# Optimization experiments

Hardware: AMD Instinct MI355X
Metric: run time of the kernel (lower is better)

## Reference

```python
import jax, jax.numpy as jnp
import numpy as np

N_NODES = 100000
N_EDGES = 3200000
IN_CH = 512
HIDDEN = 64
LOC_OUT = 16
OUT_CH = 40


def setup_inputs() -> dict:
    key = jax.random.key(0)
    ks = jax.random.split(key, 10)
    return {
        "batch_x": jax.random.normal(ks[0], (N_NODES, IN_CH), dtype=jnp.float32),
        "edge_index": jax.random.randint(ks[1], (2, N_EDGES), 0, N_NODES, dtype=jnp.int64),
        "glob_emb": jax.random.normal(ks[2], (N_NODES, LOC_OUT), dtype=jnp.float32),
        "W1": jax.random.normal(ks[3], (IN_CH, HIDDEN), dtype=jnp.float32) * (1.0 / np.sqrt(IN_CH)),
        "b1": jnp.zeros((HIDDEN,), dtype=jnp.float32),
        "W2": jax.random.normal(ks[4], (HIDDEN, LOC_OUT), dtype=jnp.float32) * (1.0 / np.sqrt(HIDDEN)),
        "b2": jnp.zeros((LOC_OUT,), dtype=jnp.float32),
        "att_w1": jax.random.normal(ks[5], (LOC_OUT, 16), dtype=jnp.float32) * 0.25,
        "att_b1": jnp.zeros((16,), dtype=jnp.float32),
        "att_w2": jax.random.normal(ks[6], (16, 1), dtype=jnp.float32) * 0.25,
        "lin1_w": jax.random.normal(ks[7], (LOC_OUT, OUT_CH), dtype=jnp.float32) * 0.25,
        "lin1_b": jnp.zeros((OUT_CH,), dtype=jnp.float32),
    }


def _gcn_conv(x, W, b, row, col, n):
    # GCNConv: out = D^-1/2 (A + I) D^-1/2 (X W) + b   (PyG default: self-loops, sym norm)
    h = x @ W
    loops = jnp.arange(n, dtype=row.dtype)
    row2 = jnp.concatenate([row, loops])  # sources (x_j)
    col2 = jnp.concatenate([col, loops])  # targets (aggregation index)
    deg = jax.ops.segment_sum(jnp.ones_like(col2, dtype=h.dtype), col2, num_segments=n)
    dinv = jax.lax.rsqrt(jnp.maximum(deg, 1.0))  # deg >= 1 thanks to self-loops
    norm = dinv[row2] * dinv[col2]               # [E+N]
    agg = jax.ops.segment_sum(h[row2] * norm[:, None], col2, num_segments=n)
    return agg + b


def reference(batch_x, edge_index, glob_emb, W1, b1, W2, b2, att_w1, att_b1, att_w2, lin1_w, lin1_b):
    n = batch_x.shape[0]
    row, col = edge_index[0], edge_index[1]
    x = _gcn_conv(batch_x, W1, b1, row, col, n)
    x = jax.nn.relu(x)  # dropout p=0.0 -> identity
    x = _gcn_conv(x, W2, b2, row, col, n)  # last layer: no relu/dropout
    z = jnp.stack([x, glob_emb], axis=1)  # [N, 2, 16]
    w = jnp.tanh(z @ att_w1 + att_b1) @ att_w2  # [N, 2, 1]
    beta = jax.nn.softmax(w, axis=1)
    emb = jnp.sum(beta * z, axis=1)  # [N, 16]
    return emb @ lin1_w + lin1_b  # [N, 40]
```

## Files before the change

kernel.cpp:

```cpp
#include <hip/hip_runtime.h>

#define N_IN 512
#define HID 64
#define NBLK 256
#define TILE 2048

typedef __attribute__((ext_vector_type(4))) float f32x4;
typedef __attribute__((ext_vector_type(8))) short bf16x8;

__device__ inline float bf2f(unsigned short s) {
    union { unsigned int u; float f; } v; v.u = ((unsigned int)s) << 16; return v.f;
}
__device__ inline unsigned short f2bf(float f) {
    union { float f; unsigned int u; } v; v.f = f;
    unsigned int u = v.u;
    return (unsigned short)((u + 0x7FFFu + ((u >> 16) & 1u)) >> 16);
}

__global__ __launch_bounds__(256) void k_histA_wt(const int* __restrict__ EI, int* __restrict__ hist,
                                                  const float* __restrict__ W1, unsigned short* __restrict__ Wt,
                                                  int E, int N, int K) {
    if (blockIdx.x >= NBLK) {
        int i = (blockIdx.x - NBLK) * 256 + threadIdx.x;
        int k = i >> 6, n = i & 63;
        Wt[n * 512 + k] = f2bf(W1[i]);
        return;
    }
    __shared__ int hs[512];
    __shared__ int sflag;
    if (threadIdx.x == 0) sflag = (EI[1] == 0 && EI[3] == 0 && EI[5] == 0 && EI[7] == 0) ? 1 : 0;
    for (int k = threadIdx.x; k < 512; k += 256) hs[k] = 0;
    __syncthreads();
    bool f = sflag != 0;
    int chunk = (E + NBLK - 1) / NBLK;
    int s = blockIdx.x * chunk, e = min(E, s + chunk);
    for (int i = s + threadIdx.x; i < e; i += 256) {
        int c = f ? ((const int2*)EI)[E + i].x : EI[E + i];
        if ((unsigned)c < (unsigned)N) atomicAdd(&hs[c >> 8], 1);
    }
    __syncthreads();
    for (int k = threadIdx.x; k < K; k += 256) hist[k * NBLK + blockIdx.x] = hs[k];
}

__global__ __launch_bounds__(256) void k_scan_a2(int* __restrict__ data, int* __restrict__ bsum, int n) {
    __shared__ int sd[256];
    int i = blockIdx.x * 256 + threadIdx.x;
    int v = (i < n) ? data[i] : 0;
    sd[threadIdx.x] = v;
    __syncthreads();
    for (int off = 1; off < 256; off <<= 1) {
        int t = 0;
        if (threadIdx.x >= (unsigned)off) t = sd[threadIdx.x - off];
        __syncthreads();
        sd[threadIdx.x] += t;
        __syncthreads();
    }
    if (i < n) data[i] = sd[threadIdx.x] - v;
    if (threadIdx.x == 255) bsum[blockIdx.x] = sd[255];
}

__global__ __launch_bounds__(512) void k_scan_b(const int* __restrict__ bsum, int* __restrict__ bexc, int nb) {
    __shared__ int sd[512];
    int t = threadIdx.x;
    int v = (t < nb) ? bsum[t] : 0;
    sd[t] = v;
    __syncthreads();
    for (int off = 1; off < 512; off <<= 1) {
        int u = 0;
        if (t >= off) u = sd[t - off];
        __syncthreads();
        sd[t] += u;
        __syncthreads();
    }
    if (t < nb) bexc[t] = sd[t] - v;
    if (t == 511) bexc[nb] = sd[511];
}

__global__ __launch_bounds__(256) void k_partB(const int* __restrict__ EI, const int* __restrict__ hist,
                                               const int* __restrict__ bexc, int* __restrict__ edges2,
                                               int E, int N, int K) {
    __shared__ int val[TILE];
    __shared__ unsigned short bkt[TILE];
    __shared__ int sorted[TILE];
    __shared__ unsigned short sbkt[TILE];
    __shared__ int cnt[512], seg[512], cur[512], gcur[512];
    __shared__ int wsum[4];
    __shared__ int sflag;
    int tid = threadIdx.x, b = blockIdx.x;
    int lane = tid & 63, wv = tid >> 6;
    if (tid == 0) sflag = (EI[1] == 0 && EI[3] == 0 && EI[5] == 0 && EI[7] == 0) ? 1 : 0;
    for (int k = tid; k < 512; k += 256) gcur[k] = (k < K) ? (bexc[k] + hist[k * NBLK + b]) : 0;
    __syncthreads();
    bool f = sflag != 0;
    int chunk = (E + NBLK - 1) / NBLK;
    int s = b * chunk, e = min(E, s + chunk);
    for (int ts = s; ts < e; ts += TILE) {
        int n = min(e - ts, TILE);
        for (int k = tid; k < 512; k += 256) cnt[k] = 0;
        __syncthreads();
        for (int i = tid; i < n; i += 256) {
            int r, c;
            if (f) { const int2* E2 = (const int2*)EI; r = E2[ts + i].x; c = E2[E + ts + i].x; }
            else   { r = EI[ts + i]; c = EI[E + ts + i]; }
            if ((unsigned)c < (unsigned)N) {
                unsigned short kb = (unsigned short)(c >> 8);
                if ((unsigned)r >= (unsigned)N) r = 0;
                val[i] = r | ((c & 255) << 20);
                bkt[i] = kb;
                atomicAdd(&cnt[kb], 1);
            } else bkt[i] = 0xFFFFu;
        }
        __syncthreads();
        int v0 = cnt[2 * tid], v1 = cnt[2 * tid + 1];
        int p = v0 + v1, pi = p;
        for (int d = 1; d < 64; d <<= 1) {
            int u = __shfl_up(pi, d, 64);
            if (lane >= d) pi += u;
        }
        if (lane == 63) wsum[wv] = pi;
        __syncthreads();
        int woff = 0, tot = 0;
        for (int q = 0; q < 4; ++q) { int t2 = wsum[q]; if (q < wv) woff += t2; tot += t2; }
        int pe = woff + pi - p;
        seg[2 * tid] = pe; seg[2 * tid + 1] = pe + v0;
        cur[2 * tid] = pe; cur[2 * tid + 1] = pe + v0;
        __syncthreads();
        for (int i = tid; i < n; i += 256) {
            unsigned short kb = bkt[i];
            if (kb != 0xFFFFu) {
                int pos = atomicAdd(&cur[kb], 1);
                sorted[pos] = val[i];
                sbkt[pos] = kb;
            }
        }
        __syncthreads();
        for (int j = tid; j < tot; j += 256) {
            int kb = sbkt[j];
            edges2[gcur[kb] + (j - seg[kb])] = sorted[j];
        }
        __syncthreads();
        for (int k = tid; k < K; k += 256) gcur[k] += cnt[k];
        __syncthreads();
    }
}

__global__ __launch_bounds__(256) void k_gemm1(const float* __restrict__ X, const unsigned short* __restrict__ Wt,
                                               unsigned short* __restrict__ H, int N) {
    int tid = threadIdx.x;
    int w = tid >> 6, lane = tid & 63;
    int m_l = lane & 15, q = lane >> 4;
    int m0 = blockIdx.x * 128 + w * 32;
    int rA0 = m0 + m_l, rA1 = m0 + 16 + m_l;
    int rc0 = rA0 < N ? rA0 : N - 1;
    int rc1 = rA1 < N ? rA1 : N - 1;
    const float* baseA0 = X + (size_t)rc0 * 512 + q * 8;
    const float* baseA1 = X + (size_t)rc1 * 512 + q * 8;
    const unsigned short* baseB = Wt + (size_t)m_l * 512 + q * 8;

    f32x4 acc[2][4] = {};
#pragma unroll 4
    for (int c = 0; c < 16; ++c) {
        int ko = c * 32;
        float4 x0a = *(const float4*)(baseA0 + ko);
        float4 x0b = *(const float4*)(baseA0 + ko + 4);
        float4 x1a = *(const float4*)(baseA1 + ko);
        float4 x1b = *(const float4*)(baseA1 + ko + 4);
        bf16x8 a0, a1;
        a0[0] = (short)f2bf(x0a.x); a0[1] = (short)f2bf(x0a.y); a0[2] = (short)f2bf(x0a.z); a0[3] = (short)f2bf(x0a.w);
        a0[4] = (short)f2bf(x0b.x); a0[5] = (short)f2bf(x0b.y); a0[6] = (short)f2bf(x0b.z); a0[7] = (short)f2bf(x0b.w);
        a1[0] = (short)f2bf(x1a.x); a1[1] = (short)f2bf(x1a.y); a1[2] = (short)f2bf(x1a.z); a1[3] = (short)f2bf(x1a.w);
        a1[4] = (short)f2bf(x1b.x); a1[5] = (short)f2bf(x1b.y); a1[6] = (short)f2bf(x1b.z); a1[7] = (short)f2bf(x1b.w);
#pragma unroll
        for (int t = 0; t < 4; ++t) {
            bf16x8 bb = *(const bf16x8*)(baseB + (size_t)t * 16 * 512 + ko);
            acc[0][t] = __builtin_amdgcn_mfma_f32_16x16x32_bf16(a0, bb, acc[0][t], 0, 0, 0);
            acc[1][t] = __builtin_amdgcn_mfma_f32_16x16x32_bf16(a1, bb, acc[1][t], 0, 0, 0);
        }
    }
#pragma unroll
    for (int h = 0; h < 2; ++h) {
#pragma unroll
        for (int rg = 0; rg < 4; ++rg) {
            int row = m0 + h * 16 + q * 4 + rg;
            if (row < N) {
#pragma unroll
                for (int t = 0; t < 4; ++t)
                    H[(size_t)row * 64 + t * 16 + m_l] = f2bf(acc[h][t][rg]);
            }
        }
    }
}

__global__ __launch_bounds__(256) void k_bucket(const int* __restrict__ bexc, const int* __restrict__ edges2,
                                                int* __restrict__ edges, int* __restrict__ start,
                                                float* __restrict__ dinv, unsigned short* __restrict__ H,
                                                int N, int K) {
    __shared__ int hist[256], sd[256], cur[256];
    __shared__ float dvs[256];
    int b = blockIdx.x, tid = threadIdx.x;
    int base = bexc[b];
    int end  = bexc[b + 1];
    hist[tid] = 0;
    __syncthreads();
    for (int i = base + tid; i < end; i += 256)
        atomicAdd(&hist[(edges2[i] >> 20) & 255], 1);
    __syncthreads();
    int v = hist[tid];
    sd[tid] = v;
    __syncthreads();
    for (int off = 1; off < 256; off <<= 1) {
        int t = 0;
        if (tid >= off) t = sd[tid - off];
        __syncthreads();
        sd[tid] += t;
        __syncthreads();
    }
    int excl = sd[tid] - v;
    cur[tid] = excl;
    int node = b * 256 + tid;
    float dvv = rsqrtf((float)(v + 1));
    dvs[tid] = dvv;
    if (node < N) {
        start[node] = base + excl;
        dinv[node] = dvv;
    }
    if (b == 0 && tid == 0) start[N] = bexc[K];
    __syncthreads();
    for (int i = base + tid; i < end; i += 256) {
        int pv = edges2[i];
        int pos = atomicAdd(&cur[(pv >> 20) & 255], 1);
        edges[base + pos] = pv & 0xFFFFF;
    }
    for (int rr = tid >> 4; rr < 256; rr += 16) {
        int n2 = b * 256 + rr;
        if (n2 < N) {
            float dv2 = dvs[rr];
            uint2* pp = (uint2*)(H + (size_t)n2 * 64 + (size_t)(tid & 15) * 4);
            uint2 vv = *pp;
            float f0 = bf2f((unsigned short)(vv.x & 0xffffu)) * dv2;
            float f1 = bf2f((unsigned short)(vv.x >> 16)) * dv2;
            float f2 = bf2f((unsigned short)(vv.y & 0xffffu)) * dv2;
            float f3 = bf2f((unsigned short)(vv.y >> 16)) * dv2;
            vv.x = (unsigned int)f2bf(f0) | ((unsigned int)f2bf(f1) << 16);
            vv.y = (unsigned int)f2bf(f2) | ((unsigned int)f2bf(f3) << 16);
            *pp = vv;
        }
    }
}

__global__ __launch_bounds__(256) void k_agg1g2(const unsigned short* __restrict__ H, const int* __restrict__ edges,
                                                const int* __restrict__ start, const float* __restrict__ dinv,
                                                const float* __restrict__ b1, const float* __restrict__ W2,
                                                unsigned short* __restrict__ H2, int N) {
    __shared__ float w2s[64 * 17];
    int tid = threadIdx.x;
    for (int i = tid; i < 1024; i += 256) { int k = i >> 4, c = i & 15; w2s[k * 17 + c] = W2[i]; }
    __syncthreads();
    int wid = blockIdx.x * 4 + (tid >> 6);
    int lane = tid & 63;
    if (wid >= N) return;
    int g = lane >> 4;
    int c4 = lane & 15;
    const size_t coff = (size_t)c4 * 4;
    float a0 = 0.f, a1 = 0.f, a2 = 0.f, a3 = 0.f;
    int s = start[wid], e = start[wid + 1];
    int i = s;
    if ((i & 3) && i < e) {
        int lim = min(e, (i + 3) & ~3);
        int j = i + g;
        if (j < lim) {
            uint2 v = *(const uint2*)(H + (size_t)edges[j] * 64 + coff);
            a0 += __uint_as_float(v.x << 16);
            a1 += __uint_as_float(v.x & 0xffff0000u);
            a2 += __uint_as_float(v.y << 16);
            a3 += __uint_as_float(v.y & 0xffff0000u);
        }
        i = lim;
    }
    for (; i + 32 <= e; i += 32) {
        int4 s0 = *(const int4*)(edges + i + g * 4);
        int4 s1 = *(const int4*)(edges + i + 16 + g * 4);
        uint2 v0 = *(const uint2*)(H + (size_t)s0.x * 64 + coff);
        uint2 v1 = *(const uint2*)(H + (size_t)s0.y * 64 + coff);
        uint2 v2 = *(const uint2*)(H + (size_t)s0.z * 64 + coff);
        uint2 v3 = *(const uint2*)(H + (size_t)s0.w * 64 + coff);
        uint2 v4 = *(const uint2*)(H + (size_t)s1.x * 64 + coff);
        uint2 v5 = *(const uint2*)(H + (size_t)s1.y * 64 + coff);
        uint2 v6 = *(const uint2*)(H + (size_t)s1.z * 64 + coff);
        uint2 v7 = *(const uint2*)(H + (size_t)s1.w * 64 + coff);
        a0 += __uint_as_float(v0.x << 16) + __uint_as_float(v1.x << 16)
            + __uint_as_float(v2.x << 16) + __uint_as_float(v3.x << 16)
            + __uint_as_float(v4.x << 16) + __uint_as_float(v5.x << 16)
            + __uint_as_float(v6.x << 16) + __uint_as_float(v7.x << 16);
        a1 += __uint_as_float(v0.x & 0xffff0000u) + __uint_as_float(v1.x & 0xffff0000u)
            + __uint_as_float(v2.x & 0xffff0000u) + __uint_as_float(v3.x & 0xffff0000u)
            + __uint_as_float(v4.x & 0xffff0000u) + __uint_as_float(v5.x & 0xffff0000u)
            + __uint_as_float(v6.x & 0xffff0000u) + __uint_as_float(v7.x & 0xffff0000u);
        a2 += __uint_as_float(v0.y << 16) + __uint_as_float(v1.y << 16)
            + __uint_as_float(v2.y << 16) + __uint_as_float(v3.y << 16)
            + __uint_as_float(v4.y << 16) + __uint_as_float(v5.y << 16)
            + __uint_as_float(v6.y << 16) + __uint_as_float(v7.y << 16);
        a3 += __uint_as_float(v0.y & 0xffff0000u) + __uint_as_float(v1.y & 0xffff0000u)
            + __uint_as_float(v2.y & 0xffff0000u) + __uint_as_float(v3.y & 0xffff0000u)
            + __uint_as_float(v4.y & 0xffff0000u) + __uint_as_float(v5.y & 0xffff0000u)
            + __uint_as_float(v6.y & 0xffff0000u) + __uint_as_float(v7.y & 0xffff0000u);
    }
    if (i + 16 <= e) {
        int4 sv = *(const int4*)(edges + i + g * 4);
        uint2 v0 = *(const uint2*)(H + (size_t)sv.x * 64 + coff);
        uint2 v1 = *(const uint2*)(H + (size_t)sv.y * 64 + coff);
        uint2 v2 = *(const uint2*)(H + (size_t)sv.z * 64 + coff);
        uint2 v3 = *(const uint2*)(H + (size_t)sv.w * 64 + coff);
        a0 += __uint_as_float(v0.x << 16) + __uint_as_float(v1.x << 16)
            + __uint_as_float(v2.x << 16) + __uint_as_float(v3.x << 16);
        a1 += __uint_as_float(v0.x & 0xffff0000u) + __uint_as_float(v1.x & 0xffff0000u)
            + __uint_as_float(v2.x & 0xffff0000u) + __uint_as_float(v3.x & 0xffff0000u);
        a2 += __uint_as_float(v0.y << 16) + __uint_as_float(v1.y << 16)
            + __uint_as_float(v2.y << 16) + __uint_as_float(v3.y << 16);
        a3 += __uint_as_float(v0.y & 0xffff0000u) + __uint_as_float(v1.y & 0xffff0000u)
            + __uint_as_float(v2.y & 0xffff0000u) + __uint_as_float(v3.y & 0xffff0000u);
        i += 16;
    }
    for (; i < e; i += 4) {
        int j = i + g;
        if (j < e) {
            uint2 v = *(const uint2*)(H + (size_t)edges[j] * 64 + coff);
            a0 += __uint_as_float(v.x << 16);
            a1 += __uint_as_float(v.x & 0xffff0000u);
            a2 += __uint_as_float(v.y << 16);
            a3 += __uint_as_float(v.y & 0xffff0000u);
        }
    }
    a0 += __shfl_xor(a0, 16, 64); a0 += __shfl_xor(a0, 32, 64);
    a1 += __shfl_xor(a1, 16, 64); a1 += __shfl_xor(a1, 32, 64);
    a2 += __shfl_xor(a2, 16, 64); a2 += __shfl_xor(a2, 32, 64);
    a3 += __shfl_xor(a3, 16, 64); a3 += __shfl_xor(a3, 32, 64);
    float dv = dinv[wid];
    uint2 sv = *(const uint2*)(H + (size_t)wid * 64 + coff);
    a0 += __uint_as_float(sv.x << 16);
    a1 += __uint_as_float(sv.x & 0xffff0000u);
    a2 += __uint_as_float(sv.y << 16);
    a3 += __uint_as_float(sv.y & 0xffff0000u);
    float4 bv = *(const float4*)(b1 + c4 * 4);
    float r0 = fmaxf(a0 * dv + bv.x, 0.f);
    float r1 = fmaxf(a1 * dv + bv.y, 0.f);
    float r2 = fmaxf(a2 * dv + bv.z, 0.f);
    float r3 = fmaxf(a3 * dv + bv.w, 0.f);
    float p = 0.f;
#pragma unroll
    for (int j = 0; j < 4; ++j) {
        int src = 4 * g + j;
        float x0 = __shfl(r0, src, 64);
        float x1 = __shfl(r1, src, 64);
        float x2 = __shfl(r2, src, 64);
        float x3 = __shfl(r3, src, 64);
        int kb = 16 * g + 4 * j;
        p += x0 * w2s[(kb + 0) * 17 + c4];
        p += x1 * w2s[(kb + 1) * 17 + c4];
        p += x2 * w2s[(kb + 2) * 17 + c4];
        p += x3 * w2s[(kb + 3) * 17 + c4];
    }
    p += __shfl_xor(p, 16, 64);
    p += __shfl_xor(p, 32, 64);
    if (g == 0) H2[(size_t)wid * 16 + c4] = f2bf(p * dv);
}

__global__ __launch_bounds__(256) void k_agg2(const unsigned short* __restrict__ H2, const int* __restrict__ edges,
                                              const int* __restrict__ start, const float* __restrict__ dinv,
                                              const float* __restrict__ b2, float* __restrict__ X2, int N) {
    int wid = blockIdx.x * 4 + (threadIdx.x >> 6);
    int lane = threadIdx.x & 63;
    if (wid >= N) return;
    int g = lane >> 3;
    int c2 = lane & 7;
    const size_t coff = (size_t)c2 * 2;
    float a0 = 0.f, a1 = 0.f;
    int s = start[wid], e = start[wid + 1];
    int i = s;
    if ((i & 3) && i < e) {
        int lim = min(e, (i + 3) & ~3);
        int j = i + g;
        if (j < lim) {
            unsigned int v = *(const unsigned int*)(H2 + (size_t)edges[j] * 16 + coff);
            a0 += __uint_as_float(v << 16);
            a1 += __uint_as_float(v & 0xffff0000u);
        }
        i = lim;
    }
    for (; i + 64 <= e; i += 64) {
        int4 s0 = *(const int4*)(edges + i + g * 4);
        int4 s1 = *(const int4*)(edges + i + 32 + g * 4);
        unsigned int v0 = *(const unsigned int*)(H2 + (size_t)s0.x * 16 + coff);
        unsigned int v1 = *(const unsigned int*)(H2 + (size_t)s0.y * 16 + coff);
        unsigned int v2 = *(const unsigned int*)(H2 + (size_t)s0.z * 16 + coff);
        unsigned int v3 = *(const unsigned int*)(H2 + (size_t)s0.w * 16 + coff);
        unsigned int v4 = *(const unsigned int*)(H2 + (size_t)s1.x * 16 + coff);
        unsigned int v5 = *(const unsigned int*)(H2 + (size_t)s1.y * 16 + coff);
        unsigned int v6 = *(const unsigned int*)(H2 + (size_t)s1.z * 16 + coff);
        unsigned int v7 = *(const unsigned int*)(H2 + (size_t)s1.w * 16 + coff);
        a0 += __uint_as_float(v0 << 16) + __uint_as_float(v1 << 16)
            + __uint_as_float(v2 << 16) + __uint_as_float(v3 << 16)
            + __uint_as_float(v4 << 16) + __uint_as_float(v5 << 16)
            + __uint_as_float(v6 << 16) + __uint_as_float(v7 << 16);
        a1 += __uint_as_float(v0 & 0xffff0000u) + __uint_as_float(v1 & 0xffff0000u)
            + __uint_as_float(v2 & 0xffff0000u) + __uint_as_float(v3 & 0xffff0000u)
            + __uint_as_float(v4 & 0xffff0000u) + __uint_as_float(v5 & 0xffff0000u)
            + __uint_as_float(v6 & 0xffff0000u) + __uint_as_float(v7 & 0xffff0000u);
    }
    if (i + 32 <= e) {
        int4 sv = *(const int4*)(edges + i + g * 4);
        unsigned int v0 = *(const unsigned int*)(H2 + (size_t)sv.x * 16 + coff);
        unsigned int v1 = *(const unsigned int*)(H2 + (size_t)sv.y * 16 + coff);
        unsigned int v2 = *(const unsigned int*)(H2 + (size_t)sv.z * 16 + coff);
        unsigned int v3 = *(const unsigned int*)(H2 + (size_t)sv.w * 16 + coff);
        a0 += __uint_as_float(v0 << 16) + __uint_as_float(v1 << 16)
            + __uint_as_float(v2 << 16) + __uint_as_float(v3 << 16);
        a1 += __uint_as_float(v0 & 0xffff0000u) + __uint_as_float(v1 & 0xffff0000u)
            + __uint_as_float(v2 & 0xffff0000u) + __uint_as_float(v3 & 0xffff0000u);
        i += 32;
    }
    for (; i < e; i += 8) {
        int j = i + g;
        if (j < e) {
            unsigned int v = *(const unsigned int*)(H2 + (size_t)edges[j] * 16 + coff);
            a0 += __uint_as_float(v << 16);
            a1 += __uint_as_float(v & 0xffff0000u);
        }
    }
    a0 += __shfl_xor(a0, 8, 64); a0 += __shfl_xor(a0, 16, 64); a0 += __shfl_xor(a0, 32, 64);
    a1 += __shfl_xor(a1, 8, 64); a1 += __shfl_xor(a1, 16, 64); a1 += __shfl_xor(a1, 32, 64);
    if (g == 0) {
        float dv = dinv[wid];
        unsigned int sv = *(const unsigned int*)(H2 + (size_t)wid * 16 + coff);
        a0 += __uint_as_float(sv << 16);
        a1 += __uint_as_float(sv & 0xffff0000u);
        float2 bv = *(const float2*)(b2 + c2 * 2);
        float2 o; o.x = a0 * dv + bv.x; o.y = a1 * dv + bv.y;
        *(float2*)(X2 + (size_t)wid * 16 + coff) = o;
    }
}

__global__ __launch_bounds__(256) void k_head(const float* __restrict__ X2, const float* __restrict__ G,
                                              const float* __restrict__ AW1, const float* __restrict__ AB1,
                                              const float* __restrict__ AW2, const float* __restrict__ LW,
                                              const float* __restrict__ LB, float* __restrict__ OUT, int N) {
    __shared__ float s_aw1[256], s_ab1[16], s_aw2[16], s_lw[640], s_lb[40];
    int tid = threadIdx.x;
    s_aw1[tid] = AW1[tid];
    if (tid < 16) { s_ab1[tid] = AB1[tid]; s_aw2[tid] = AW2[tid]; }
    for (int i = tid; i < 640; i += 256) s_lw[i] = LW[i];
    if (tid < 40) s_lb[tid] = LB[tid];
    __syncthreads();
    int node = blockIdx.x * 256 + tid;
    if (node >= N) return;
    float x[16], g[16];
    const float4* xp = (const float4*)(X2 + (size_t)node * 16);
    const float4* gp = (const float4*)(G + (size_t)node * 16);
#pragma unroll
    for (int q = 0; q < 4; ++q) {
        float4 v = xp[q]; x[q*4] = v.x; x[q*4+1] = v.y; x[q*4+2] = v.z; x[q*4+3] = v.w;
        float4 u = gp[q]; g[q*4] = u.x; g[q*4+1] = u.y; g[q*4+2] = u.z; g[q*4+3] = u.w;
    }
    float wx = 0.f, wg = 0.f;
#pragma unroll
    for (int j = 0; j < 16; ++j) {
        float tx = s_ab1[j], tg = s_ab1[j];
#pragma unroll
        for (int c = 0; c < 16; ++c) { tx += x[c] * s_aw1[c*16 + j]; tg += g[c] * s_aw1[c*16 + j]; }
        wx += tanhf(tx) * s_aw2[j];
        wg += tanhf(tg) * s_aw2[j];
    }
    float m = fmaxf(wx, wg);
    float ex = expf(wx - m), eg = expf(wg - m);
    float inv = 1.f / (ex + eg);
    float bx = ex * inv, bg = eg * inv;
    float emb[16];
#pragma unroll
    for (int c = 0; c < 16; ++c) emb[c] = bx * x[c] + bg * g[c];
    float* op = OUT + (size_t)node * 40;
    for (int o = 0; o < 40; ++o) {
        float a = s_lb[o];
#pragma unroll
        for (int c = 0; c < 16; ++c) a += emb[c] * s_lw[c*40 + o];
        op[o] = a;
    }
}

extern "C" void kernel_launch(void* const* d_in, const int* in_sizes, int n_in,
                              void* d_out, int out_size, void* d_ws, size_t ws_size,
                              hipStream_t stream) {
    const float* X   = (const float*)d_in[0];
    const int*   EI  = (const int*)d_in[1];
    const float* G   = (const float*)d_in[2];
    const float* W1  = (const float*)d_in[3];
    const float* B1  = (const float*)d_in[4];
    const float* W2  = (const float*)d_in[5];
    const float* B2  = (const float*)d_in[6];
    const float* AW1 = (const float*)d_in[7];
    const float* AB1 = (const float*)d_in[8];
    const float* AW2 = (const float*)d_in[9];
    const float* LW  = (const float*)d_in[10];
    const float* LB  = (const float*)d_in[11];
    float* OUT = (float*)d_out;

    const int N = in_sizes[0] / N_IN;
    const int E = in_sizes[1] / 2;
    const int NB = (N + 255) / 256;
    const int K  = NB;
    const int NH = K * NBLK;
    const int SB = (NH + 255) / 256;
    const int WB = (N_IN * HID + 255) / 256;
    const int GB = (N + 127) / 128;

    char* w = (char*)d_ws;
    size_t off = 0;
    auto take = [&](size_t bytes) -> void* {
        void* p = (void*)(w + off);
        off = (off + bytes + 255) & ~(size_t)255;
        return p;
    };
    int*   hist   = (int*)take((size_t)NH * 4);
    int*   bsum   = (int*)take((size_t)SB * 4);
    int*   bexc   = (int*)take((size_t)(SB + 1) * 4);
    int*   startp = (int*)take((size_t)(N + 1) * 4);
    float* dinvp  = (float*)take((size_t)N * 4);
    int*   edges2 = (int*)take((size_t)E * 4);
    int*   edges  = (int*)take((size_t)E * 4);
    unsigned short* wt = (unsigned short*)take((size_t)N_IN * HID * 2);
    unsigned short* h1 = (unsigned short*)take((size_t)N * 64 * 2);
    unsigned short* h2 = (unsigned short*)take((size_t)N * 16 * 2);
    float* x2 = (float*)take((size_t)N * 16 * 4);
    (void)ws_size; (void)n_in; (void)out_size;

    k_histA_wt<<<NBLK + WB, 256, 0, stream>>>(EI, hist, W1, wt, E, N, K);
    k_scan_a2 <<<SB, 256, 0, stream>>>(hist, bsum, NH);
    k_scan_b  <<<1, 512, 0, stream>>>(bsum, bexc, SB);
    k_partB   <<<NBLK, 256, 0, stream>>>(EI, hist, bexc, edges2, E, N, K);
    k_gemm1   <<<GB, 256, 0, stream>>>(X, wt, h1, N);
    k_bucket  <<<K, 256, 0, stream>>>(bexc, edges2, edges, startp, dinvp, h1, N, K);
    k_agg1g2  <<<(N + 3) / 4, 256, 0, stream>>>(h1, edges, startp, dinvp, B1, W2, h2, N);
    k_agg2    <<<(N + 3) / 4, 256, 0, stream>>>(h2, edges, startp, dinvp, B2, x2, N);
    k_head    <<<NB, 256, 0, stream>>>(x2, G, AW1, AB1, AW2, LW, LB, OUT, N);
}
```

Baseline: 613.1 us.

## Replace tiled local sort in edge partition with direct atomic scatter

```diff
diff --git a/kernel.cpp b/kernel.cpp
--- a/kernel.cpp
+++ b/kernel.cpp
@@ -3,7 +3,6 @@
 #define N_IN 512
 #define HID 64
 #define NBLK 256
-#define TILE 2048
 
 typedef __attribute__((ext_vector_type(4))) float f32x4;
 typedef __attribute__((ext_vector_type(8))) short bf16x8;
@@ -17,29 +16,32 @@
     return (unsigned short)((u + 0x7FFFu + ((u >> 16) & 1u)) >> 16);
 }
 
-__global__ __launch_bounds__(256) void k_histA_wt(const int* __restrict__ EI, int* __restrict__ hist,
-                                                  const float* __restrict__ W1, unsigned short* __restrict__ Wt,
-                                                  int E, int N, int K) {
+__global__ __launch_bounds__(1024) void k_histA_wt(const int* __restrict__ EI, int* __restrict__ hist,
+                                                   const float* __restrict__ W1, unsigned short* __restrict__ Wt,
+                                                   int E, int N, int K) {
+    int tid = threadIdx.x;
     if (blockIdx.x >= NBLK) {
-        int i = (blockIdx.x - NBLK) * 256 + threadIdx.x;
-        int k = i >> 6, n = i & 63;
-        Wt[n * 512 + k] = f2bf(W1[i]);
+        int i = (blockIdx.x - NBLK) * 1024 + tid;
+        if (i < N_IN * HID) {
+            int k = i >> 6, n = i & 63;
+            Wt[n * 512 + k] = f2bf(W1[i]);
+        }
         return;
     }
     __shared__ int hs[512];
     __shared__ int sflag;
-    if (threadIdx.x == 0) sflag = (EI[1] == 0 && EI[3] == 0 && EI[5] == 0 && EI[7] == 0) ? 1 : 0;
-    for (int k = threadIdx.x; k < 512; k += 256) hs[k] = 0;
+    if (tid == 0) sflag = (EI[1] == 0 && EI[3] == 0 && EI[5] == 0 && EI[7] == 0) ? 1 : 0;
+    if (tid < 512) hs[tid] = 0;
     __syncthreads();
     bool f = sflag != 0;
     int chunk = (E + NBLK - 1) / NBLK;
     int s = blockIdx.x * chunk, e = min(E, s + chunk);
-    for (int i = s + threadIdx.x; i < e; i += 256) {
+    for (int i = s + tid; i < e; i += 1024) {
         int c = f ? ((const int2*)EI)[E + i].x : EI[E + i];
         if ((unsigned)c < (unsigned)N) atomicAdd(&hs[c >> 8], 1);
     }
     __syncthreads();
-    for (int k = threadIdx.x; k < K; k += 256) hist[k * NBLK + blockIdx.x] = hs[k];
+    for (int k = tid; k < K; k += 1024) hist[k * NBLK + blockIdx.x] = hs[k];
 }
 
 __global__ __launch_bounds__(256) void k_scan_a2(int* __restrict__ data, int* __restrict__ bsum, int n) {
@@ -76,71 +78,25 @@
     if (t == 511) bexc[nb] = sd[511];
 }
 
-__global__ __launch_bounds__(256) void k_partB(const int* __restrict__ EI, const int* __restrict__ hist,
-                                               const int* __restrict__ bexc, int* __restrict__ edges2,
-                                               int E, int N, int K) {
-    __shared__ int val[TILE];
-    __shared__ unsigned short bkt[TILE];
-    __shared__ int sorted[TILE];
-    __shared__ unsigned short sbkt[TILE];
-    __shared__ int cnt[512], seg[512], cur[512], gcur[512];
-    __shared__ int wsum[4];
+__global__ __launch_bounds__(1024) void k_partB(const int* __restrict__ EI, const int* __restrict__ hist,
+                                                const int* __restrict__ bexc, int* __restrict__ edges2,
+                                                int E, int N, int K) {
+    __shared__ int cur[512];
     __shared__ int sflag;
     int tid = threadIdx.x, b = blockIdx.x;
-    int lane = tid & 63, wv = tid >> 6;
     if (tid == 0) sflag = (EI[1] == 0 && EI[3] == 0 && EI[5] == 0 && EI[7] == 0) ? 1 : 0;
-    for (int k = tid; k < 512; k += 256) gcur[k] = (k < K) ? (bexc[k] + hist[k * NBLK + b]) : 0;
+    if (tid < 512) cur[tid] = (tid < K) ? (bexc[tid] + hist[tid * NBLK + b]) : 0;
     __syncthreads();
     bool f = sflag != 0;
     int chunk = (E + NBLK - 1) / NBLK;
     int s = b * chunk, e = min(E, s + chunk);
-    for (int ts = s; ts < e; ts += TILE) {
-        int n = min(e - ts, TILE);
-        for (int k = tid; k < 512; k += 256) cnt[k] = 0;
-        __syncthreads();
-        for (int i = tid; i < n; i += 256) {
-            int r, c;
-            if (f) { const int2* E2 = (const int2*)EI; r = E2[ts + i].x; c = E2[E + ts + i].x; }
-            else   { r = EI[ts + i]; c = EI[E + ts + i]; }
-            if ((unsigned)c < (unsigned)N) {
-                unsigned short kb = (unsigned short)(c >> 8);
-                if ((unsigned)r >= (unsigned)N) r = 0;
-                val[i] = r | ((c & 255) << 20);
-                bkt[i] = kb;
-                atomicAdd(&cnt[kb], 1);
-            } else bkt[i] = 0xFFFFu;
-        }
-        __syncthreads();
-        int v0 = cnt[2 * tid], v1 = cnt[2 * tid + 1];
-        int p = v0 + v1, pi = p;
-        for (int d = 1; d < 64; d <<= 1) {
-            int u = __shfl_up(pi, d, 64);
-            if (lane >= d) pi += u;
-        }
-        if (lane == 63) wsum[wv] = pi;
-        __syncthreads();
-        int woff = 0, tot = 0;
-        for (int q = 0; q < 4; ++q) { int t2 = wsum[q]; if (q < wv) woff += t2; tot += t2; }
-        int pe = woff + pi - p;
-        seg[2 * tid] = pe; seg[2 * tid + 1] = pe + v0;
-        cur[2 * tid] = pe; cur[2 * tid + 1] = pe + v0;
-        __syncthreads();
-        for (int i = tid; i < n; i += 256) {
-            unsigned short kb = bkt[i];
-            if (kb != 0xFFFFu) {
-                int pos = atomicAdd(&cur[kb], 1);
-                sorted[pos] = val[i];
-                sbkt[pos] = kb;
-            }
-        }
-        __syncthreads();
-        for (int j = tid; j < tot; j += 256) {
-            int kb = sbkt[j];
-            edges2[gcur[kb] + (j - seg[kb])] = sorted[j];
-        }
-        __syncthreads();
-        for (int k = tid; k < K; k += 256) gcur[k] += cnt[k];
-        __syncthreads();
+    for (int i = s + tid; i < e; i += 1024) {
+        int r, c;
+        if (f) { const int2* E2 = (const int2*)EI; r = E2[i].x; c = E2[E + i].x; }
+        else   { r = EI[i]; c = EI[E + i]; }
+        if ((unsigned)r >= (unsigned)N || (unsigned)c >= (unsigned)N) continue;
+        int pos = atomicAdd(&cur[c >> 8], 1);
+        edges2[pos] = r | ((c & 255) << 20);
     }
 }
 
@@ -509,7 +465,7 @@
     const int K  = NB;
     const int NH = K * NBLK;
     const int SB = (NH + 255) / 256;
-    const int WB = (N_IN * HID + 255) / 256;
+    const int WB = (N_IN * HID + 1023) / 1024;
     const int GB = (N + 127) / 128;
 
     char* w = (char*)d_ws;
@@ -532,10 +488,10 @@
     float* x2 = (float*)take((size_t)N * 16 * 4);
     (void)ws_size; (void)n_in; (void)out_size;
 
-    k_histA_wt<<<NBLK + WB, 256, 0, stream>>>(EI, hist, W1, wt, E, N, K);
+    k_histA_wt<<<NBLK + WB, 1024, 0, stream>>>(EI, hist, W1, wt, E, N, K);
     k_scan_a2 <<<SB, 256, 0, stream>>>(hist, bsum, NH);
     k_scan_b  <<<1, 512, 0, stream>>>(bsum, bexc, SB);
-    k_partB   <<<NBLK, 256, 0, stream>>>(EI, hist, bexc, edges2, E, N, K);
+    k_partB   <<<NBLK, 1024, 0, stream>>>(EI, hist, bexc, edges2, E, N, K);
     k_gemm1   <<<GB, 256, 0, stream>>>(X, wt, h1, N);
     k_bucket  <<<K, 256, 0, stream>>>(bexc, edges2, edges, startp, dinvp, h1, N, K);
     k_agg1g2  <<<(N + 3) / 4, 256, 0, stream>>>(h1, edges, startp, dinvp, B1, W2, h2, N);
```

Result: faster. 571.8 us (-6.7%).
